# Optimization experiments

Hardware: AMD Instinct MI355X
Metric: run time of the kernel (lower is better)

## Reference

```python
import jax, jax.numpy as jnp
import numpy as np

NUM_BINS = 15
NUM_CLASSES = 4
NEIGHBORHOOD_WIDTH = 3  # K; num_neighbor_classes = K**2 = 9


def _neighbor_counts(onehot):
    """Count of same-class neighbors in KxK window (center excluded), zero padding.
    onehot: [B, C, H, W] float32 one-hot of hard predictions.
    returns int32 [B, C, H, W] in [0, K^2-1].
    """
    K = NEIGHBORHOOD_WIDTH
    C = onehot.shape[1]
    kern = np.ones((K, K), dtype=np.float32)
    kern[K // 2, K // 2] = 0.0  # exclude center pixel
    kernel = jnp.asarray(np.broadcast_to(kern, (C, 1, K, K)).copy())  # depthwise OIHW
    counts = jax.lax.conv_general_dilated(
        onehot, kernel,
        window_strides=(1, 1), padding='SAME',
        feature_group_count=C,
        dimension_numbers=('NCHW', 'OIHW', 'NCHW'))
    return jnp.clip(jnp.round(counts).astype(jnp.int32), 0, K * K - 1)


def setup_inputs() -> dict:
    key = jax.random.key(0)
    k1, k2 = jax.random.split(key)
    logits = jax.random.normal(k1, (16, NUM_CLASSES, 512, 512), dtype=jnp.float32)
    # calibration frequency table: val_freqs[class][neighbor_count][conf_bin]
    val_freqs = jax.random.uniform(k2, (NUM_CLASSES, NEIGHBORHOOD_WIDTH ** 2, NUM_BINS), dtype=jnp.float32)
    return {"logits": logits, "val_freqs": val_freqs}


def reference(logits, val_freqs):
    B, C, H, W = logits.shape
    probs = jax.nn.softmax(logits, axis=1)                      # [B,C,H,W]
    y_hard = jnp.argmax(probs, axis=1)                          # [B,H,W]

    # (y_hard == lab_idx) for every class at once -> one-hot [B,C,H,W]
    onehot = jax.nn.one_hot(y_hard, C, axis=1, dtype=jnp.float32)
    agg = _neighbor_counts(onehot)                              # [B,C,H,W] int32 in [0, K^2-1]

    # confidence bin per pixel/class: uniform bins on [0,1]
    bin_width = 1.0 / NUM_BINS
    bin_map = jnp.clip((probs / bin_width).astype(jnp.int32), 0, NUM_BINS - 1)  # [B,C,H,W]

    # fused multi-index gather replacing the nested class/neighbor-mask loops:
    # calibrated[b,c,h,w] = val_freqs[c, agg[b,c,h,w], bin_map[b,c,h,w]]
    cls_idx = jnp.arange(C, dtype=jnp.int32)[None, :, None, None]
    calibrated = val_freqs[cls_idx, agg, bin_map]               # [B,C,H,W]

    # normalize across classes, guarding zero sums
    s = jnp.sum(calibrated, axis=1, keepdims=True)
    s = jnp.where(s == 0, 1.0, s)
    return calibrated / s
```

## Files before the change

kernel.cpp:

```cpp
#include <hip/hip_runtime.h>

#define HW (512 * 512)

typedef float vfloat4 __attribute__((ext_vector_type(4)));

constexpr int TX = 64, TY = 16;
constexpr int CWP = 67;
constexpr float BWIDTH = 1.0f / 15.0f;
constexpr float DELTA = 3e-5f;

__global__ __launch_bounds__(256) void nectar_binning_kernel(
    const float* __restrict__ logits,
    const float* __restrict__ val_freqs,
    float* __restrict__ out)
{
    __shared__ unsigned int cls[18 * CWP];
    __shared__ float vf[540];

    const int b  = blockIdx.z;
    const int w0 = blockIdx.x * TX;
    const int h0 = blockIdx.y * TY;
    const int tid = threadIdx.x;

    for (int i = tid; i < 540; i += 256) vf[i] = val_freqs[i];

    const float* lb = logits + (size_t)b * 4 * HW;

    const int tix = tid & 15;
    const int tiy = tid >> 4;
    const int w = w0 + 4 * tix;
    const int h = h0 + tiy;
    const int base = (h << 9) + w;

    float xv[4][4];
    #pragma unroll
    for (int c = 0; c < 4; c++) {
        vfloat4 v = *reinterpret_cast<const vfloat4*>(lb + (size_t)c * HW + base);
        xv[c][0] = v.x; xv[c][1] = v.y; xv[c][2] = v.z; xv[c][3] = v.w;
    }

    unsigned int pbin[4];
    #pragma unroll
    for (int j = 0; j < 4; j++) {
        float x0 = xv[0][j], x1 = xv[1][j], x2 = xv[2][j], x3 = xv[3][j];
        int c = 0; float best = x0;
        if (x1 > best) { best = x1; c = 1; }
        if (x2 > best) { best = x2; c = 2; }
        if (x3 > best) { best = x3; c = 3; }
        cls[(tiy + 1) * CWP + 1 + 4 * tix + j] = 1u << (4 * c);

        float m = fmaxf(fmaxf(x0, x1), fmaxf(x2, x3));
        float t0 = x0 - m, t1 = x1 - m, t2 = x2 - m, t3 = x3 - m;
        float f0 = __expf(t0), f1 = __expf(t1), f2 = __expf(t2), f3 = __expf(t3);
        float sf = ((f0 + f1) + f2) + f3;
        float rs = __builtin_amdgcn_rcpf(sf);
        float q[4];
        q[0] = (f0 * rs) * 15.0f; q[1] = (f1 * rs) * 15.0f;
        q[2] = (f2 * rs) * 15.0f; q[3] = (f3 * rs) * 15.0f;
        bool slow = false;
        #pragma unroll
        for (int c2 = 0; c2 < 4; c2++) {
            float fr = q[c2] - floorf(q[c2]);
            slow |= (fr < DELTA) | (fr > 1.0f - DELTA);
        }
        if (slow) {
            float e0 = expf(t0), e1 = expf(t1), e2 = expf(t2), e3 = expf(t3);
            float s = ((e0 + e1) + e2) + e3;
            q[0] = (e0 / s) / BWIDTH; q[1] = (e1 / s) / BWIDTH;
            q[2] = (e2 / s) / BWIDTH; q[3] = (e3 / s) / BWIDTH;
        }
        unsigned int pb = 0;
        #pragma unroll
        for (int c2 = 0; c2 < 4; c2++) {
            int bin = (int)q[c2];
            bin = bin > 14 ? 14 : bin;
            pb |= (unsigned int)bin << (4 * c2);
        }
        pbin[j] = pb;
    }

    if (tid < 164) {
        int ly, lx;
        if (tid < 66)       { ly = 0;        lx = tid;       }
        else if (tid < 132) { ly = 17;       lx = tid - 66;  }
        else if (tid < 148) { ly = tid - 131; lx = 0;        }
        else                { ly = tid - 147; lx = 65;       }
        int hh = h0 + ly - 1;
        int ww = w0 + lx - 1;
        unsigned int v = 0;
        if ((unsigned)hh < 512u && (unsigned)ww < 512u) {
            int bb = (hh << 9) + ww;
            float x0 = lb[bb];
            float x1 = lb[HW + bb];
            float x2 = lb[2 * HW + bb];
            float x3 = lb[3 * HW + bb];
            int c = 0; float best = x0;
            if (x1 > best) { best = x1; c = 1; }
            if (x2 > best) { best = x2; c = 2; }
            if (x3 > best) { best = x3; c = 3; }
            v = 1u << (4 * c);
        }
        cls[ly * CWP + lx] = v;
    }
    __syncthreads();

    const unsigned int* p0 = &cls[tiy * CWP + 4 * tix];
    unsigned int r1[6], colsum[6];
    #pragma unroll
    for (int j = 0; j < 6; j++) {
        unsigned int a = p0[j];
        unsigned int bmid = p0[CWP + j];
        unsigned int cbot = p0[2 * CWP + j];
        r1[j] = bmid;
        colsum[j] = a + bmid + cbot;
    }

    float res[4][4];
    #pragma unroll
    for (int j = 0; j < 4; j++) {
        unsigned int pk = colsum[j] + colsum[j + 1] + colsum[j + 2] - r1[j + 1];
        unsigned int pb = pbin[j];
        float cs = 0.0f;
        float cal[4];
        #pragma unroll
        for (int c = 0; c < 4; c++) {
            int cnt = (int)((pk >> (4 * c)) & 0xFu);
            int bin = (int)((pb >> (4 * c)) & 0xFu);
            float v = vf[c * 135 + cnt * 15 + bin];
            cal[c] = v;
            cs += v;
        }
        if (cs == 0.0f) cs = 1.0f;
        float inv = __builtin_amdgcn_rcpf(cs);
        #pragma unroll
        for (int c = 0; c < 4; c++) res[c][j] = cal[c] * inv;
    }

    float* ob = out + (size_t)b * 4 * HW + base;
    #pragma unroll
    for (int c = 0; c < 4; c++) {
        vfloat4 v;
        v.x = res[c][0]; v.y = res[c][1]; v.z = res[c][2]; v.w = res[c][3];
        __builtin_nontemporal_store(v, reinterpret_cast<vfloat4*>(ob + (size_t)c * HW));
    }
}

extern "C" void kernel_launch(void* const* d_in, const int* in_sizes, int n_in,
                              void* d_out, int out_size, void* d_ws, size_t ws_size,
                              hipStream_t stream) {
    const float* logits    = (const float*)d_in[0];
    const float* val_freqs = (const float*)d_in[1];
    float* out             = (float*)d_out;

    dim3 block(256, 1, 1);
    dim3 grid(512 / TX, 512 / TY, 16);
    hipLaunchKernelGGL(nectar_binning_kernel, grid, block, 0, stream,
                       logits, val_freqs, out);
}
```

Before: 116.4 us.

## Process two row strips per thread with taller tiles and early halo loads

Each thread now handles two 4-pixel groups sixteen rows apart, so a block covers a 64x32 tile instead of 64x16. This halves the halo overhead per output pixel and the number of blocks. All logit loads, including the halo ring, are issued up front to increase memory-level parallelism. The cost is higher register pressure and fewer blocks, which may lower occupancy.

```diff
diff --git a/kernel.cpp b/kernel.cpp
--- a/kernel.cpp
+++ b/kernel.cpp
@@ -4,7 +4,7 @@
 
 typedef float vfloat4 __attribute__((ext_vector_type(4)));
 
-constexpr int TX = 64, TY = 16;
+constexpr int TX = 64, TY = 32;
 constexpr int CWP = 67;
 constexpr float BWIDTH = 1.0f / 15.0f;
 constexpr float DELTA = 3e-5f;
@@ -14,7 +14,7 @@
     const float* __restrict__ val_freqs,
     float* __restrict__ out)
 {
-    __shared__ unsigned int cls[18 * CWP];
+    __shared__ unsigned int cls[34 * CWP];
     __shared__ float vf[540];
 
     const int b  = blockIdx.z;
@@ -29,25 +29,47 @@
     const int tix = tid & 15;
     const int tiy = tid >> 4;
     const int w = w0 + 4 * tix;
-    const int h = h0 + tiy;
-    const int base = (h << 9) + w;
+    const int hA = h0 + tiy;
+    const int baseA = (hA << 9) + w;
+    const int baseB = baseA + (16 << 9);
 
-    float xv[4][4];
+    vfloat4 xa[4], xb[4];
     #pragma unroll
-    for (int c = 0; c < 4; c++) {
-        vfloat4 v = *reinterpret_cast<const vfloat4*>(lb + (size_t)c * HW + base);
-        xv[c][0] = v.x; xv[c][1] = v.y; xv[c][2] = v.z; xv[c][3] = v.w;
+    for (int c = 0; c < 4; c++)
+        xa[c] = *reinterpret_cast<const vfloat4*>(lb + (size_t)c * HW + baseA);
+    #pragma unroll
+    for (int c = 0; c < 4; c++)
+        xb[c] = *reinterpret_cast<const vfloat4*>(lb + (size_t)c * HW + baseB);
+
+    float r0 = 0.f, r1 = 0.f, r2 = 0.f, r3 = 0.f;
+    int ringdst = 0;
+    bool ringv = false;
+    if (tid < 196) {
+        int ly, lx;
+        if (tid < 66)       { ly = 0;         lx = tid;       }
+        else if (tid < 132) { ly = 33;        lx = tid - 66;  }
+        else if (tid < 164) { ly = tid - 131; lx = 0;         }
+        else                { ly = tid - 163; lx = 65;        }
+        ringdst = ly * CWP + lx;
+        int hh = h0 + ly - 1;
+        int ww = w0 + lx - 1;
+        if ((unsigned)hh < 512u && (unsigned)ww < 512u) {
+            ringv = true;
+            int bb = (hh << 9) + ww;
+            r0 = lb[bb];
+            r1 = lb[HW + bb];
+            r2 = lb[2 * HW + bb];
+            r3 = lb[3 * HW + bb];
+        }
     }
 
-    unsigned int pbin[4];
-    #pragma unroll
-    for (int j = 0; j < 4; j++) {
-        float x0 = xv[0][j], x1 = xv[1][j], x2 = xv[2][j], x3 = xv[3][j];
+    auto px_phase1 = [&](float x0, float x1, float x2, float x3,
+                         int clsaddr) -> unsigned int {
         int c = 0; float best = x0;
         if (x1 > best) { best = x1; c = 1; }
         if (x2 > best) { best = x2; c = 2; }
         if (x3 > best) { best = x3; c = 3; }
-        cls[(tiy + 1) * CWP + 1 + 4 * tix + j] = 1u << (4 * c);
+        cls[clsaddr] = 1u << (4 * c);
 
         float m = fmaxf(fmaxf(x0, x1), fmaxf(x2, x3));
         float t0 = x0 - m, t1 = x1 - m, t2 = x2 - m, t3 = x3 - m;
@@ -76,73 +98,75 @@
             bin = bin > 14 ? 14 : bin;
             pb |= (unsigned int)bin << (4 * c2);
         }
-        pbin[j] = pb;
-    }
+        return pb;
+    };
 
-    if (tid < 164) {
-        int ly, lx;
-        if (tid < 66)       { ly = 0;        lx = tid;       }
-        else if (tid < 132) { ly = 17;       lx = tid - 66;  }
-        else if (tid < 148) { ly = tid - 131; lx = 0;        }
-        else                { ly = tid - 147; lx = 65;       }
-        int hh = h0 + ly - 1;
-        int ww = w0 + lx - 1;
+    unsigned int pbinA[4], pbinB[4];
+    #pragma unroll
+    for (int j = 0; j < 4; j++)
+        pbinA[j] = px_phase1(xa[0][j], xa[1][j], xa[2][j], xa[3][j],
+                             (tiy + 1) * CWP + 1 + 4 * tix + j);
+    #pragma unroll
+    for (int j = 0; j < 4; j++)
+        pbinB[j] = px_phase1(xb[0][j], xb[1][j], xb[2][j], xb[3][j],
+                             (tiy + 17) * CWP + 1 + 4 * tix + j);
+
+    if (tid < 196) {
         unsigned int v = 0;
-        if ((unsigned)hh < 512u && (unsigned)ww < 512u) {
-            int bb = (hh << 9) + ww;
-            float x0 = lb[bb];
-            float x1 = lb[HW + bb];
-            float x2 = lb[2 * HW + bb];
-            float x3 = lb[3 * HW + bb];
-            int c = 0; float best = x0;
-            if (x1 > best) { best = x1; c = 1; }
-            if (x2 > best) { best = x2; c = 2; }
-            if (x3 > best) { best = x3; c = 3; }
+        if (ringv) {
+            int c = 0; float best = r0;
+            if (r1 > best) { best = r1; c = 1; }
+            if (r2 > best) { best = r2; c = 2; }
+            if (r3 > best) { best = r3; c = 3; }
             v = 1u << (4 * c);
         }
-        cls[ly * CWP + lx] = v;
+        cls[ringdst] = v;
     }
     __syncthreads();
 
-    const unsigned int* p0 = &cls[tiy * CWP + 4 * tix];
-    unsigned int r1[6], colsum[6];
-    #pragma unroll
-    for (int j = 0; j < 6; j++) {
-        unsigned int a = p0[j];
-        unsigned int bmid = p0[CWP + j];
-        unsigned int cbot = p0[2 * CWP + j];
-        r1[j] = bmid;
-        colsum[j] = a + bmid + cbot;
-    }
+    auto strip_phase2 = [&](int row0, const unsigned int* pbin, float* ob) {
+        const unsigned int* p0 = &cls[row0 * CWP + 4 * tix];
+        unsigned int r1v[6], colsum[6];
+        #pragma unroll
+        for (int j = 0; j < 6; j++) {
+            unsigned int a    = p0[j];
+            unsigned int bmid = p0[CWP + j];
+            unsigned int cbot = p0[2 * CWP + j];
+            r1v[j] = bmid;
+            colsum[j] = a + bmid + cbot;
+        }
 
-    float res[4][4];
-    #pragma unroll
-    for (int j = 0; j < 4; j++) {
-        unsigned int pk = colsum[j] + colsum[j + 1] + colsum[j + 2] - r1[j + 1];
-        unsigned int pb = pbin[j];
-        float cs = 0.0f;
-        float cal[4];
+        float res[4][4];
+        #pragma unroll
+        for (int j = 0; j < 4; j++) {
+            unsigned int pk = colsum[j] + colsum[j + 1] + colsum[j + 2] - r1v[j + 1];
+            unsigned int pb = pbin[j];
+            float cs = 0.0f;
+            float cal[4];
+            #pragma unroll
+            for (int c = 0; c < 4; c++) {
+                int cnt = (int)((pk >> (4 * c)) & 0xFu);
+                int bin = (int)((pb >> (4 * c)) & 0xFu);
+                float v = vf[c * 135 + cnt * 15 + bin];
+                cal[c] = v;
+                cs += v;
+            }
+            if (cs == 0.0f) cs = 1.0f;
+            float inv = __builtin_amdgcn_rcpf(cs);
+            #pragma unroll
+            for (int c = 0; c < 4; c++) res[c][j] = cal[c] * inv;
+        }
         #pragma unroll
         for (int c = 0; c < 4; c++) {
-            int cnt = (int)((pk >> (4 * c)) & 0xFu);
-            int bin = (int)((pb >> (4 * c)) & 0xFu);
-            float v = vf[c * 135 + cnt * 15 + bin];
-            cal[c] = v;
-            cs += v;
+            vfloat4 v;
+            v.x = res[c][0]; v.y = res[c][1]; v.z = res[c][2]; v.w = res[c][3];
+            __builtin_nontemporal_store(v, reinterpret_cast<vfloat4*>(ob + (size_t)c * HW));
         }
-        if (cs == 0.0f) cs = 1.0f;
-        float inv = __builtin_amdgcn_rcpf(cs);
-        #pragma unroll
-        for (int c = 0; c < 4; c++) res[c][j] = cal[c] * inv;
-    }
+    };
 
-    float* ob = out + (size_t)b * 4 * HW + base;
-    #pragma unroll
-    for (int c = 0; c < 4; c++) {
-        vfloat4 v;
-        v.x = res[c][0]; v.y = res[c][1]; v.z = res[c][2]; v.w = res[c][3];
-        __builtin_nontemporal_store(v, reinterpret_cast<vfloat4*>(ob + (size_t)c * HW));
-    }
+    float* obase = out + (size_t)b * 4 * HW;
+    strip_phase2(tiy,      pbinA, obase + baseA);
+    strip_phase2(tiy + 16, pbinB, obase + baseB);
 }
 
 extern "C" void kernel_launch(void* const* d_in, const int* in_sizes, int n_in,
```

After: 119.0 us. +2.3%, slower.

## Use full-width 4-row panels with vectorized halo loads and XCD-aware block mapping

Applied to the files above, without the earlier changes.

Each block now covers a full 512-wide strip of four rows with 512 threads, in place of 64x16 tiles. Left and right halos vanish, so only the top and bottom halo rows are loaded, as coalesced float2 vectors by every thread instead of scattered scalar loads. Block indices are swizzled so that consecutive panels of a batch land on the same XCD, and the LDS neighbor reads become uint4 vector loads. The cost is a larger halo-to-interior ratio, since each 4-row panel still loads two extra rows, which raises redundant global reads compared with 16-row tiles.

```diff
diff --git a/kernel.cpp b/kernel.cpp
--- a/kernel.cpp
+++ b/kernel.cpp
@@ -3,51 +3,64 @@
 #define HW (512 * 512)
 
 typedef float vfloat4 __attribute__((ext_vector_type(4)));
+typedef float vfloat2 __attribute__((ext_vector_type(2)));
+typedef unsigned int vuint4 __attribute__((ext_vector_type(4)));
 
-constexpr int TX = 64, TY = 16;
-constexpr int CWP = 67;
+constexpr int CWP = 516;
 constexpr float BWIDTH = 1.0f / 15.0f;
 constexpr float DELTA = 3e-5f;
 
-__global__ __launch_bounds__(256) void nectar_binning_kernel(
+__global__ __launch_bounds__(512) void nectar_binning_kernel(
     const float* __restrict__ logits,
     const float* __restrict__ val_freqs,
     float* __restrict__ out)
 {
-    __shared__ unsigned int cls[18 * CWP];
+    __shared__ unsigned int cls[6 * CWP];
     __shared__ float vf[540];
 
-    const int b  = blockIdx.z;
-    const int w0 = blockIdx.x * TX;
-    const int h0 = blockIdx.y * TY;
-    const int tid = threadIdx.x;
+    const unsigned int f = blockIdx.x;
+    const unsigned int l = ((f & 7u) << 8) | (f >> 3);
+    const int panel = (int)(l & 127u);
+    const int b     = (int)(l >> 7);
+    const int h0  = panel * 4;
+    const int tid = (int)threadIdx.x;
 
-    for (int i = tid; i < 540; i += 256) vf[i] = val_freqs[i];
+    for (int i = tid; i < 540; i += 512) vf[i] = val_freqs[i];
+    if (tid < 6) { cls[tid * CWP] = 0u; cls[tid * CWP + 513] = 0u; }
 
     const float* lb = logits + (size_t)b * 4 * HW;
 
-    const int tix = tid & 15;
-    const int tiy = tid >> 4;
-    const int w = w0 + 4 * tix;
-    const int h = h0 + tiy;
-    const int base = (h << 9) + w;
+    const int r = tid >> 7;
+    const int t = tid & 127;
+    const int w = 4 * t;
+    const int base = ((h0 + r) << 9) + w;
 
-    float xv[4][4];
+    vfloat4 xa[4];
     #pragma unroll
-    for (int c = 0; c < 4; c++) {
-        vfloat4 v = *reinterpret_cast<const vfloat4*>(lb + (size_t)c * HW + base);
-        xv[c][0] = v.x; xv[c][1] = v.y; xv[c][2] = v.z; xv[c][3] = v.w;
+    for (int c = 0; c < 4; c++)
+        xa[c] = *reinterpret_cast<const vfloat4*>(lb + (size_t)c * HW + base);
+
+    const int hrow = tid >> 8;
+    const int p = tid & 255;
+    const int hh = hrow ? (h0 + 4) : (h0 - 1);
+    const bool hv = (unsigned)hh < 512u;
+    vfloat2 hx[4];
+    #pragma unroll
+    for (int c = 0; c < 4; c++) { hx[c].x = 0.f; hx[c].y = 0.f; }
+    if (hv) {
+        const int hb = (hh << 9) + 2 * p;
+        #pragma unroll
+        for (int c = 0; c < 4; c++)
+            hx[c] = *reinterpret_cast<const vfloat2*>(lb + (size_t)c * HW + hb);
     }
 
-    unsigned int pbin[4];
-    #pragma unroll
-    for (int j = 0; j < 4; j++) {
-        float x0 = xv[0][j], x1 = xv[1][j], x2 = xv[2][j], x3 = xv[3][j];
+    auto px_phase1 = [&](float x0, float x1, float x2, float x3,
+                         int clsaddr) -> unsigned int {
         int c = 0; float best = x0;
         if (x1 > best) { best = x1; c = 1; }
         if (x2 > best) { best = x2; c = 2; }
         if (x3 > best) { best = x3; c = 3; }
-        cls[(tiy + 1) * CWP + 1 + 4 * tix + j] = 1u << (4 * c);
+        cls[clsaddr] = 1u << (4 * c);
 
         float m = fmaxf(fmaxf(x0, x1), fmaxf(x2, x3));
         float t0 = x0 - m, t1 = x1 - m, t2 = x2 - m, t3 = x3 - m;
@@ -76,49 +89,56 @@
             bin = bin > 14 ? 14 : bin;
             pb |= (unsigned int)bin << (4 * c2);
         }
-        pbin[j] = pb;
-    }
+        return pb;
+    };
 
-    if (tid < 164) {
-        int ly, lx;
-        if (tid < 66)       { ly = 0;        lx = tid;       }
-        else if (tid < 132) { ly = 17;       lx = tid - 66;  }
-        else if (tid < 148) { ly = tid - 131; lx = 0;        }
-        else                { ly = tid - 147; lx = 65;       }
-        int hh = h0 + ly - 1;
-        int ww = w0 + lx - 1;
-        unsigned int v = 0;
-        if ((unsigned)hh < 512u && (unsigned)ww < 512u) {
-            int bb = (hh << 9) + ww;
-            float x0 = lb[bb];
-            float x1 = lb[HW + bb];
-            float x2 = lb[2 * HW + bb];
-            float x3 = lb[3 * HW + bb];
-            int c = 0; float best = x0;
-            if (x1 > best) { best = x1; c = 1; }
-            if (x2 > best) { best = x2; c = 2; }
-            if (x3 > best) { best = x3; c = 3; }
-            v = 1u << (4 * c);
+    unsigned int pbin[4];
+    #pragma unroll
+    for (int j = 0; j < 4; j++)
+        pbin[j] = px_phase1(xa[0][j], xa[1][j], xa[2][j], xa[3][j],
+                            (r + 1) * CWP + 1 + w + j);
+
+    {
+        unsigned int v0 = 0, v1 = 0;
+        if (hv) {
+            int c = 0; float best = hx[0].x;
+            if (hx[1].x > best) { best = hx[1].x; c = 1; }
+            if (hx[2].x > best) { best = hx[2].x; c = 2; }
+            if (hx[3].x > best) { best = hx[3].x; c = 3; }
+            v0 = 1u << (4 * c);
+            c = 0; best = hx[0].y;
+            if (hx[1].y > best) { best = hx[1].y; c = 1; }
+            if (hx[2].y > best) { best = hx[2].y; c = 2; }
+            if (hx[3].y > best) { best = hx[3].y; c = 3; }
+            v1 = 1u << (4 * c);
         }
-        cls[ly * CWP + lx] = v;
+        const int hl = hrow * 5 * CWP + 1 + 2 * p;
+        cls[hl]     = v0;
+        cls[hl + 1] = v1;
     }
     __syncthreads();
 
-    const unsigned int* p0 = &cls[tiy * CWP + 4 * tix];
-    unsigned int r1[6], colsum[6];
+    const unsigned int* p0 = &cls[r * CWP + w];
+    vuint4 ra[3], rb[3];
     #pragma unroll
-    for (int j = 0; j < 6; j++) {
-        unsigned int a = p0[j];
-        unsigned int bmid = p0[CWP + j];
-        unsigned int cbot = p0[2 * CWP + j];
-        r1[j] = bmid;
-        colsum[j] = a + bmid + cbot;
+    for (int k = 0; k < 3; k++) {
+        ra[k] = *reinterpret_cast<const vuint4*>(p0 + k * CWP);
+        rb[k] = *reinterpret_cast<const vuint4*>(p0 + k * CWP + 4);
+    }
+    unsigned int colsum[6], mid[6];
+    #pragma unroll
+    for (int k = 0; k < 6; k++) {
+        unsigned int a0 = (k < 4) ? ra[0][k] : rb[0][k - 4];
+        unsigned int a1 = (k < 4) ? ra[1][k] : rb[1][k - 4];
+        unsigned int a2 = (k < 4) ? ra[2][k] : rb[2][k - 4];
+        mid[k] = a1;
+        colsum[k] = a0 + a1 + a2;
     }
 
     float res[4][4];
     #pragma unroll
     for (int j = 0; j < 4; j++) {
-        unsigned int pk = colsum[j] + colsum[j + 1] + colsum[j + 2] - r1[j + 1];
+        unsigned int pk = colsum[j] + colsum[j + 1] + colsum[j + 2] - mid[j + 1];
         unsigned int pb = pbin[j];
         float cs = 0.0f;
         float cal[4];
@@ -152,8 +172,8 @@
     const float* val_freqs = (const float*)d_in[1];
     float* out             = (float*)d_out;
 
-    dim3 block(256, 1, 1);
-    dim3 grid(512 / TX, 512 / TY, 16);
+    dim3 block(512, 1, 1);
+    dim3 grid(2048, 1, 1);
     hipLaunchKernelGGL(nectar_binning_kernel, grid, block, 0, stream,
                        logits, val_freqs, out);
 }
```

Result: faster. 110.9 us (-4.7%).

## Stream row strips per wavefront with register rotation and shuffle-based halos

Applied to the files above, without the earlier changes.

Each wavefront now processes a strip of 4 full-width rows. It loads the next row while computing the current one, and keeps the packed per-row class nibbles in rotating registers. Horizontal neighbour sums come from cross-lane shuffles instead of a shared-memory class tile, which removes the scalar halo loads and the block-wide barrier. The block index is swizzled, and the lookup table is copied to shared memory by every wave. In exchange, the one-row halo above and below each 4-row strip is re-read, and the grid has far fewer, longer-lived waves, which may lower occupancy and memory-level parallelism.

```diff
diff --git a/kernel.cpp b/kernel.cpp
--- a/kernel.cpp
+++ b/kernel.cpp
@@ -4,8 +4,6 @@
 
 typedef float vfloat4 __attribute__((ext_vector_type(4)));
 
-constexpr int TX = 64, TY = 16;
-constexpr int CWP = 67;
 constexpr float BWIDTH = 1.0f / 15.0f;
 constexpr float DELTA = 3e-5f;
 
@@ -14,135 +12,205 @@
     const float* __restrict__ val_freqs,
     float* __restrict__ out)
 {
-    __shared__ unsigned int cls[18 * CWP];
     __shared__ float vf[540];
 
-    const int b  = blockIdx.z;
-    const int w0 = blockIdx.x * TX;
-    const int h0 = blockIdx.y * TY;
-    const int tid = threadIdx.x;
-
-    for (int i = tid; i < 540; i += 256) vf[i] = val_freqs[i];
+    const int tid  = (int)threadIdx.x;
+    const int lane = tid & 63;
+    const int wv   = tid >> 6;
+
+    float vfr[9];
+    #pragma unroll
+    for (int i = 0; i < 9; i++) {
+        int idx = 64 * i + lane;
+        vfr[i] = (idx < 540) ? val_freqs[idx] : 0.f;
+    }
+
+    const unsigned bi  = blockIdx.x;
+    const unsigned bsw = ((bi & 7u) << 6) | (bi >> 3);
+    const int seg = (int)(4u * bsw) + wv;
+    const int b   = seg >> 7;
+    const int grp = seg & 127;
+    const int h0  = grp << 2;
 
     const float* lb = logits + (size_t)b * 4 * HW;
-
-    const int tix = tid & 15;
-    const int tiy = tid >> 4;
-    const int w = w0 + 4 * tix;
-    const int h = h0 + tiy;
-    const int base = (h << 9) + w;
-
-    float xv[4][4];
+    float*       ob = out    + (size_t)b * 4 * HW;
+    const int colA = 4 * lane;
+    const int colB = 256 + 4 * lane;
+
+    auto LOADROW = [&](vfloat4 (&dst)[4][2], int r) {
+        const float* rp = lb + (r << 9);
+        #pragma unroll
+        for (int c = 0; c < 4; c++) {
+            dst[c][0] = *reinterpret_cast<const vfloat4*>(rp + (size_t)c * HW + colA);
+            dst[c][1] = *reinterpret_cast<const vfloat4*>(rp + (size_t)c * HW + colB);
+        }
+    };
+
+    auto NIBROW = [&](const vfloat4 (&x)[4][2], unsigned (&N)[2][2]) {
+        #pragma unroll
+        for (int h = 0; h < 2; h++) {
+            unsigned n[4];
+            #pragma unroll
+            for (int j = 0; j < 4; j++) {
+                float x0 = x[0][h][j], x1 = x[1][h][j], x2 = x[2][h][j], x3 = x[3][h][j];
+                int c = 0; float best = x0;
+                if (x1 > best) { best = x1; c = 1; }
+                if (x2 > best) { best = x2; c = 2; }
+                if (x3 > best) { best = x3; c = 3; }
+                n[j] = 1u << (4 * c);
+            }
+            N[h][0] = n[0] | (n[1] << 16);
+            N[h][1] = n[2] | (n[3] << 16);
+        }
+    };
+
+    auto NIBPBROW = [&](const vfloat4 (&x)[4][2], unsigned (&N)[2][2], unsigned (&P)[2][2]) {
+        #pragma unroll
+        for (int h = 0; h < 2; h++) {
+            unsigned n[4], pbv[4];
+            #pragma unroll
+            for (int j = 0; j < 4; j++) {
+                float x0 = x[0][h][j], x1 = x[1][h][j], x2 = x[2][h][j], x3 = x[3][h][j];
+                int c = 0; float best = x0;
+                if (x1 > best) { best = x1; c = 1; }
+                if (x2 > best) { best = x2; c = 2; }
+                if (x3 > best) { best = x3; c = 3; }
+                n[j] = 1u << (4 * c);
+
+                float m = fmaxf(fmaxf(x0, x1), fmaxf(x2, x3));
+                float t0 = x0 - m, t1 = x1 - m, t2 = x2 - m, t3 = x3 - m;
+                float f0 = __expf(t0), f1 = __expf(t1), f2 = __expf(t2), f3 = __expf(t3);
+                float sf = ((f0 + f1) + f2) + f3;
+                float rs = __builtin_amdgcn_rcpf(sf);
+                float q[4];
+                q[0] = (f0 * rs) * 15.0f; q[1] = (f1 * rs) * 15.0f;
+                q[2] = (f2 * rs) * 15.0f; q[3] = (f3 * rs) * 15.0f;
+                bool slow = false;
+                #pragma unroll
+                for (int c2 = 0; c2 < 4; c2++) {
+                    float fr = q[c2] - floorf(q[c2]);
+                    slow |= (fr < DELTA) | (fr > 1.0f - DELTA);
+                }
+                if (slow) {
+                    float e0 = expf(t0), e1 = expf(t1), e2 = expf(t2), e3 = expf(t3);
+                    float s = ((e0 + e1) + e2) + e3;
+                    q[0] = (e0 / s) / BWIDTH; q[1] = (e1 / s) / BWIDTH;
+                    q[2] = (e2 / s) / BWIDTH; q[3] = (e3 / s) / BWIDTH;
+                }
+                unsigned pb = 0;
+                #pragma unroll
+                for (int c2 = 0; c2 < 4; c2++) {
+                    int bin = (int)q[c2];
+                    bin = bin > 14 ? 14 : bin;
+                    pb |= (unsigned)bin << (4 * c2);
+                }
+                pbv[j] = pb;
+            }
+            N[h][0] = n[0]   | (n[1]   << 16);
+            N[h][1] = n[2]   | (n[3]   << 16);
+            P[h][0] = pbv[0] | (pbv[1] << 16);
+            P[h][1] = pbv[2] | (pbv[3] << 16);
+        }
+    };
+
+    auto OUTROW = [&](int r, const unsigned (&T)[2][2], const unsigned (&M)[2][2],
+                      const unsigned (&B)[2][2], const unsigned (&P)[2][2]) {
+        unsigned C[2][2];
+        #pragma unroll
+        for (int h = 0; h < 2; h++) {
+            C[h][0] = T[h][0] + M[h][0] + B[h][0];
+            C[h][1] = T[h][1] + M[h][1] + B[h][1];
+        }
+        unsigned upA = __shfl_up(C[0][1], 1) >> 16;   if (lane == 0)  upA = 0;
+        unsigned ebA = __shfl(C[0][1], 63) >> 16;
+        unsigned upB = __shfl_up(C[1][1], 1) >> 16;   if (lane == 0)  upB = ebA;
+        unsigned e0B = __shfl(C[1][0], 0) & 0xFFFFu;
+        unsigned dnA = __shfl_down(C[0][0], 1) & 0xFFFFu; if (lane == 63) dnA = e0B;
+        unsigned dnB = __shfl_down(C[1][0], 1) & 0xFFFFu; if (lane == 63) dnB = 0;
+        const unsigned up[2] = {upA, upB}, dn[2] = {dnA, dnB};
+
+        float res[4][2][4];
+        #pragma unroll
+        for (int h = 0; h < 2; h++) {
+            unsigned L0 = (C[h][0] << 16) | up[h];
+            unsigned R0 = (C[h][0] >> 16) | (C[h][1] << 16);
+            unsigned R1 = (C[h][1] >> 16) | (dn[h] << 16);
+            unsigned PKw[2];
+            PKw[0] = C[h][0] + L0 + R0 - M[h][0];
+            PKw[1] = C[h][1] + R0 + R1 - M[h][1];
+            #pragma unroll
+            for (int j = 0; j < 4; j++) {
+                unsigned pk = (PKw[j >> 1]  >> (16 * (j & 1))) & 0xFFFFu;
+                unsigned pb = (P[h][j >> 1] >> (16 * (j & 1))) & 0xFFFFu;
+                float cs = 0.0f;
+                float cal[4];
+                #pragma unroll
+                for (int c = 0; c < 4; c++) {
+                    int cnt = (int)((pk >> (4 * c)) & 0xFu);
+                    int bin = (int)((pb >> (4 * c)) & 0xFu);
+                    float v = vf[c * 135 + cnt * 15 + bin];
+                    cal[c] = v;
+                    cs += v;
+                }
+                if (cs == 0.0f) cs = 1.0f;
+                float inv = __builtin_amdgcn_rcpf(cs);
+                #pragma unroll
+                for (int c = 0; c < 4; c++) res[c][h][j] = cal[c] * inv;
+            }
+        }
+        float* rp = ob + (r << 9);
+        #pragma unroll
+        for (int c = 0; c < 4; c++) {
+            vfloat4 v0; v0.x = res[c][0][0]; v0.y = res[c][0][1]; v0.z = res[c][0][2]; v0.w = res[c][0][3];
+            vfloat4 v1; v1.x = res[c][1][0]; v1.y = res[c][1][1]; v1.z = res[c][1][2]; v1.w = res[c][1][3];
+            __builtin_nontemporal_store(v0, reinterpret_cast<vfloat4*>(rp + (size_t)c * HW + colA));
+            __builtin_nontemporal_store(v1, reinterpret_cast<vfloat4*>(rp + (size_t)c * HW + colB));
+        }
+    };
+
+    auto ROT = [&](unsigned (&T)[2][2], unsigned (&M)[2][2], const unsigned (&B)[2][2],
+                   unsigned (&PC)[2][2], const unsigned (&PN)[2][2]) {
+        #pragma unroll
+        for (int h = 0; h < 2; h++)
+            #pragma unroll
+            for (int k = 0; k < 2; k++) {
+                T[h][k] = M[h][k]; M[h][k] = B[h][k]; PC[h][k] = PN[h][k];
+            }
+    };
+
+    vfloat4 U[4][2], V[4][2];
+    unsigned T[2][2], M[2][2], B[2][2], PC[2][2], PN[2][2];
+
+    LOADROW(U, (grp > 0) ? (h0 - 1) : 0);
+    LOADROW(V, h0);
     #pragma unroll
-    for (int c = 0; c < 4; c++) {
-        vfloat4 v = *reinterpret_cast<const vfloat4*>(lb + (size_t)c * HW + base);
-        xv[c][0] = v.x; xv[c][1] = v.y; xv[c][2] = v.z; xv[c][3] = v.w;
+    for (int i = 0; i < 9; i++) {
+        int idx = 64 * i + lane;
+        if (idx < 540) vf[idx] = vfr[i];
     }
-
-    unsigned int pbin[4];
-    #pragma unroll
-    for (int j = 0; j < 4; j++) {
-        float x0 = xv[0][j], x1 = xv[1][j], x2 = xv[2][j], x3 = xv[3][j];
-        int c = 0; float best = x0;
-        if (x1 > best) { best = x1; c = 1; }
-        if (x2 > best) { best = x2; c = 2; }
-        if (x3 > best) { best = x3; c = 3; }
-        cls[(tiy + 1) * CWP + 1 + 4 * tix + j] = 1u << (4 * c);
-
-        float m = fmaxf(fmaxf(x0, x1), fmaxf(x2, x3));
-        float t0 = x0 - m, t1 = x1 - m, t2 = x2 - m, t3 = x3 - m;
-        float f0 = __expf(t0), f1 = __expf(t1), f2 = __expf(t2), f3 = __expf(t3);
-        float sf = ((f0 + f1) + f2) + f3;
-        float rs = __builtin_amdgcn_rcpf(sf);
-        float q[4];
-        q[0] = (f0 * rs) * 15.0f; q[1] = (f1 * rs) * 15.0f;
-        q[2] = (f2 * rs) * 15.0f; q[3] = (f3 * rs) * 15.0f;
-        bool slow = false;
-        #pragma unroll
-        for (int c2 = 0; c2 < 4; c2++) {
-            float fr = q[c2] - floorf(q[c2]);
-            slow |= (fr < DELTA) | (fr > 1.0f - DELTA);
-        }
-        if (slow) {
-            float e0 = expf(t0), e1 = expf(t1), e2 = expf(t2), e3 = expf(t3);
-            float s = ((e0 + e1) + e2) + e3;
-            q[0] = (e0 / s) / BWIDTH; q[1] = (e1 / s) / BWIDTH;
-            q[2] = (e2 / s) / BWIDTH; q[3] = (e3 / s) / BWIDTH;
-        }
-        unsigned int pb = 0;
-        #pragma unroll
-        for (int c2 = 0; c2 < 4; c2++) {
-            int bin = (int)q[c2];
-            bin = bin > 14 ? 14 : bin;
-            pb |= (unsigned int)bin << (4 * c2);
-        }
-        pbin[j] = pb;
-    }
-
-    if (tid < 164) {
-        int ly, lx;
-        if (tid < 66)       { ly = 0;        lx = tid;       }
-        else if (tid < 132) { ly = 17;       lx = tid - 66;  }
-        else if (tid < 148) { ly = tid - 131; lx = 0;        }
-        else                { ly = tid - 147; lx = 65;       }
-        int hh = h0 + ly - 1;
-        int ww = w0 + lx - 1;
-        unsigned int v = 0;
-        if ((unsigned)hh < 512u && (unsigned)ww < 512u) {
-            int bb = (hh << 9) + ww;
-            float x0 = lb[bb];
-            float x1 = lb[HW + bb];
-            float x2 = lb[2 * HW + bb];
-            float x3 = lb[3 * HW + bb];
-            int c = 0; float best = x0;
-            if (x1 > best) { best = x1; c = 1; }
-            if (x2 > best) { best = x2; c = 2; }
-            if (x3 > best) { best = x3; c = 3; }
-            v = 1u << (4 * c);
-        }
-        cls[ly * CWP + lx] = v;
-    }
-    __syncthreads();
-
-    const unsigned int* p0 = &cls[tiy * CWP + 4 * tix];
-    unsigned int r1[6], colsum[6];
-    #pragma unroll
-    for (int j = 0; j < 6; j++) {
-        unsigned int a = p0[j];
-        unsigned int bmid = p0[CWP + j];
-        unsigned int cbot = p0[2 * CWP + j];
-        r1[j] = bmid;
-        colsum[j] = a + bmid + cbot;
-    }
-
-    float res[4][4];
-    #pragma unroll
-    for (int j = 0; j < 4; j++) {
-        unsigned int pk = colsum[j] + colsum[j + 1] + colsum[j + 2] - r1[j + 1];
-        unsigned int pb = pbin[j];
-        float cs = 0.0f;
-        float cal[4];
-        #pragma unroll
-        for (int c = 0; c < 4; c++) {
-            int cnt = (int)((pk >> (4 * c)) & 0xFu);
-            int bin = (int)((pb >> (4 * c)) & 0xFu);
-            float v = vf[c * 135 + cnt * 15 + bin];
-            cal[c] = v;
-            cs += v;
-        }
-        if (cs == 0.0f) cs = 1.0f;
-        float inv = __builtin_amdgcn_rcpf(cs);
-        #pragma unroll
-        for (int c = 0; c < 4; c++) res[c][j] = cal[c] * inv;
-    }
-
-    float* ob = out + (size_t)b * 4 * HW + base;
-    #pragma unroll
-    for (int c = 0; c < 4; c++) {
-        vfloat4 v;
-        v.x = res[c][0]; v.y = res[c][1]; v.z = res[c][2]; v.w = res[c][3];
-        __builtin_nontemporal_store(v, reinterpret_cast<vfloat4*>(ob + (size_t)c * HW));
-    }
+    NIBROW(U, T);
+    if (grp == 0) { T[0][0] = T[0][1] = T[1][0] = T[1][1] = 0; }
+    LOADROW(U, h0 + 1);
+    NIBPBROW(V, M, PC);
+    LOADROW(V, h0 + 2);
+
+    NIBPBROW(U, B, PN);
+    LOADROW(U, h0 + 3);
+    OUTROW(h0, T, M, B, PC);
+    ROT(T, M, B, PC, PN);
+
+    NIBPBROW(V, B, PN);
+    LOADROW(V, (grp < 127) ? (h0 + 4) : 511);
+    OUTROW(h0 + 1, T, M, B, PC);
+    ROT(T, M, B, PC, PN);
+
+    NIBPBROW(U, B, PN);
+    OUTROW(h0 + 2, T, M, B, PC);
+    ROT(T, M, B, PC, PN);
+
+    NIBROW(V, B);
+    if (grp == 127) { B[0][0] = B[0][1] = B[1][0] = B[1][1] = 0; }
+    OUTROW(h0 + 3, T, M, B, PC);
 }
 
 extern "C" void kernel_launch(void* const* d_in, const int* in_sizes, int n_in,
@@ -153,7 +221,7 @@
     float* out             = (float*)d_out;
 
     dim3 block(256, 1, 1);
-    dim3 grid(512 / TX, 512 / TY, 16);
+    dim3 grid(512, 1, 1);
     hipLaunchKernelGGL(nectar_binning_kernel, grid, block, 0, stream,
                        logits, val_freqs, out);
 }
```

Result: no change. 114.6 us (-1.5%).
